# Optimization experiments

Measured on AMD Instinct MI355X. Metric: run time of the kernel, lower is better.

The kernel has to match this reference:

```python
import jax, jax.numpy as jnp
import numpy as np

B = 4096
D_IN = 1024
H1 = 2048
H2 = 1024
E = 7          # num_experts, forced by broadcasting in source
T = 2          # num_tasks
NS = 7         # scene dimension of S
EMB_ROWS = 10
EMB_DIM = 16


def setup_inputs() -> dict:
    key = jax.random.key(0)
    ks = jax.random.split(key, 8)
    x = jax.random.normal(ks[0], (B, D_IN), dtype=jnp.float32)
    scene = jax.random.randint(ks[1], (B,), 0, E)
    # Expert MLP params, stacked over experts: Linear(D_IN->H1)+ReLU, Linear(H1->H2)+ReLU
    W1 = jax.random.normal(ks[2], (E, D_IN, H1), dtype=jnp.float32) * (1.0 / np.sqrt(D_IN))
    b1 = jnp.zeros((E, H1), dtype=jnp.float32)
    W2 = jax.random.normal(ks[3], (E, H1, H2), dtype=jnp.float32) * (1.0 / np.sqrt(H1))
    b2 = jnp.zeros((E, H2), dtype=jnp.float32)
    # Routing tensor S: [7, input_dim+16, num_experts] (xavier-like init)
    S = jax.random.normal(ks[4], (NS, D_IN + EMB_DIM, E), dtype=jnp.float32) * 0.02
    scene_emb = jax.random.normal(ks[5], (EMB_ROWS, EMB_DIM), dtype=jnp.float32)
    return {"x": x, "scene": scene, "W1": W1, "b1": b1, "W2": W2, "b2": b2,
            "S": S, "scene_emb": scene_emb}


def _forward(x, scene, W1, b1, W2, b2, S, scene_emb):
    # Experts (vectorized over the E expert MLPs): [B,E,H2]
    h = jax.nn.relu(jnp.einsum('bd,edh->beh', x, W1) + b1)
    experts_out = jax.nn.relu(jnp.einsum('beh,eho->beo', h, W2) + b2)

    se = scene_emb[scene]                       # [B,16]
    xc = jnp.concatenate([x, se], axis=-1)      # [B, D_IN+16]
    G = jnp.einsum('bd,sde->bse', xc, S)        # [B, 7, E]
    G = jnp.transpose(G, (0, 2, 1))             # [B, E, 7]
    G = jax.nn.softmax(G, axis=-1)

    logG = jnp.log(G)                           # [B, E, 7]
    q = jnp.sum(jnp.log(G * 7.0) / 7.0, axis=-1)  # [B, E]

    KG = jnp.eye(E, dtype=x.dtype)
    ses = KG[scene][:, None, :]                 # [B, 1, E]

    _, pi = jax.lax.top_k(jnp.sum(ses * logG, axis=-1), 6)  # [B,6]
    _, qi = jax.lax.top_k(q, 6)                              # [B,6]
    select = ((KG[pi].sum(axis=1) + KG[qi].sum(axis=1)) > 0).astype(x.dtype)  # [B,E]

    gate = jax.nn.softmax(jnp.sum(G * ses, axis=-1), axis=-1) * select  # [B,E]
    out = jnp.einsum('be,bed->bd', gate, experts_out)                    # [B,H2]
    # self.gate ModuleList is unused in the source forward; each task output is identical
    return jnp.stack([out] * T, axis=0)         # [T, B, H2]


def reference(x, scene, W1, b1, W2, b2, S, scene_emb):
    return _forward(x, scene, W1, b1, W2, b2, S, scene_emb)
```

## Files before the change

kernel.cpp:

```cpp
#include <hip/hip_runtime.h>
#include <hip/hip_bf16.h>

typedef unsigned short u16;
typedef __bf16 bf8 __attribute__((ext_vector_type(8)));
typedef float f4 __attribute__((ext_vector_type(4)));

__device__ __forceinline__ u16 f2bf(float f) {
    unsigned int u = __float_as_uint(f);
    u = (u + 0x7fffu + ((u >> 16) & 1u)) >> 16;
    return (u16)u;
}

__device__ __forceinline__ void gload16(const u16* g, u16* l) {
    __builtin_amdgcn_global_load_lds((const __attribute__((address_space(1))) void*)g,
                                     (__attribute__((address_space(3))) void*)l, 16, 0, 0);
}

__global__ void cvt_x_kernel(const float* __restrict__ in, u16* __restrict__ out, int n4) {
    int i = blockIdx.x * blockDim.x + threadIdx.x;
    int stride = gridDim.x * blockDim.x;
    for (; i < n4; i += stride) {
        float4 v = ((const float4*)in)[i];
        ushort4 o;
        o.x = f2bf(v.x); o.y = f2bf(v.y); o.z = f2bf(v.z); o.w = f2bf(v.w);
        ((ushort4*)out)[i] = o;
    }
}

__global__ void transpose_cvt_kernel(const float* __restrict__ in, u16* __restrict__ out,
                                     int R, int C) {
    __shared__ u16 t[64][71];
    int e = blockIdx.z;
    int c0 = blockIdx.x * 64, r0 = blockIdx.y * 64;
    int tid = threadIdx.x;
    const float* ip = in + (size_t)e * R * C;
    u16* op = out + (size_t)e * R * C;
#pragma unroll
    for (int k = 0; k < 16; ++k) {
        int idx = k * 256 + tid;
        int r = idx >> 6, c = idx & 63;
        t[c][r] = f2bf(ip[(size_t)(r0 + r) * C + c0 + c]);
    }
    __syncthreads();
#pragma unroll
    for (int k = 0; k < 8; ++k) {
        int c = k * 8 + (tid >> 5);
        int rr = (tid & 31) * 2;
        ushort2 v = make_ushort2(t[c][rr], t[c][rr + 1]);
        *(ushort2*)(op + (size_t)(c0 + c) * R + r0 + rr) = v;
    }
}

__global__ void transpose_S_kernel(const float* __restrict__ S, float* __restrict__ ST) {
    int idx = blockIdx.x * 256 + threadIdx.x;
    if (idx >= 1040 * 52) return;
    int d = idx / 52, c = idx % 52;
    ST[idx] = (c < 49) ? S[(c / 7) * 7280 + d * 7 + (c % 7)] : 0.f;
}

__global__ void gating_kernel(const float* __restrict__ x, const int* __restrict__ scene,
                              const float* __restrict__ ST, const float* __restrict__ semb,
                              float* __restrict__ gate) {
    __shared__ float xc[4][1040];
    __shared__ float Lsh[4][49];
    int wv = threadIdx.x >> 6, lane = threadIdx.x & 63;
    int row = blockIdx.x * 4 + wv;
    float* xcw = xc[wv];
    const float* xr = x + (size_t)row * 1024;
    for (int d = lane; d < 1024; d += 64) xcw[d] = xr[d];
    int sc = scene[row];
    if (lane < 16) xcw[1024 + lane] = semb[sc * 16 + lane];
    __syncthreads();

    if (lane < 49) {
        const float* STp = ST + lane;
        float a0 = 0.f, a1 = 0.f, a2 = 0.f, a3 = 0.f;
        for (int d = 0; d < 1040; d += 4) {
            a0 += xcw[d]     * STp[d * 52];
            a1 += xcw[d + 1] * STp[d * 52 + 52];
            a2 += xcw[d + 2] * STp[d * 52 + 104];
            a3 += xcw[d + 3] * STp[d * 52 + 156];
        }
        Lsh[wv][lane] = (a0 + a1) + (a2 + a3);
    }
    __syncthreads();

    if (lane == 0) {
        float logG[7][7], Gsc[7], piS[7], qS[7];
        for (int e = 0; e < 7; e++) {
            float L[7];
            float m = -1e30f;
            for (int s = 0; s < 7; s++) { L[s] = Lsh[wv][s * 7 + e]; m = fmaxf(m, L[s]); }
            float sum = 0.f;
            for (int s = 0; s < 7; s++) sum += expf(L[s] - m);
            float lse = m + logf(sum);
            float qs = 0.f;
            for (int s = 0; s < 7; s++) { logG[e][s] = L[s] - lse; qs += logG[e][s]; }
            piS[e] = logG[e][sc];
            qS[e] = qs;
            Gsc[e] = expf(logG[e][sc]);
        }
        int epi = 0, eqi = 0; float bp = piS[0], bq = qS[0];
        for (int e = 1; e < 7; e++) {
            if (piS[e] <= bp) { bp = piS[e]; epi = e; }
            if (qS[e]  <= bq) { bq = qS[e];  eqi = e; }
        }
        float mg = -1e30f;
        for (int e = 0; e < 7; e++) mg = fmaxf(mg, Gsc[e]);
        float sum = 0.f;
        float ex[7];
        for (int e = 0; e < 7; e++) { ex[e] = expf(Gsc[e] - mg); sum += ex[e]; }
        float inv = 1.f / sum;
        for (int e = 0; e < 7; e++) {
            float g = ex[e] * inv;
            if (e == epi && e == eqi) g = 0.f;
            gate[row * 7 + e] = g;
        }
    }
}

template<bool G2>
__global__ __launch_bounds__(512, 2) void gemm8p_kernel(
    const u16* __restrict__ Abase, const u16* __restrict__ Bbase,
    const float* __restrict__ bias, const float* __restrict__ gate,
    void* __restrict__ outp)
{
    constexpr int M = 4096;
    constexpr int K = G2 ? 2048 : 1024;
    constexpr int N = G2 ? 1024 : 2048;
    constexpr int NT = K / 64;
    constexpr int LOG2NT = G2 ? 5 : 4;

    extern __shared__ u16 lds[];

    const int tid = threadIdx.x;
    const int lane = tid & 63;
    const int wid = tid >> 6;
    const int wr = wid >> 2, wc = wid & 3;
    const int ln15 = lane & 15, lnk = (lane >> 4) * 8;

    int bm, bn, e0, nE, grp;
    if constexpr (G2) {
        int id = blockIdx.x;
        int xcd = id & 7, slot = id >> 3;
        grp = xcd & 1;
        bn = slot & 3;
        bm = (slot >> 2) * 4 + (xcd >> 1);
        e0 = grp * 4; nE = grp ? 3 : 4;
    } else {
        int id = blockIdx.x;
        e0 = id >> 8;
        bm = (id & 255) >> 3;
        bn = id & 7;
        nE = 1; grp = 0;
    }
    const int NTtot = nE * NT;

    const int sr = tid >> 3;
    const int sc = (tid & 7) * 8;

    auto stageA = [&](int gt, int buf) {
#pragma unroll
        for (int l = 0; l < 2; ++l) {
            int r = l * 64 + sr;
            int cs = sc ^ ((r & 7) << 3);
            const u16* g = Abase + (G2 ? (size_t)(e0 + (gt >> LOG2NT)) * M * K : (size_t)0)
                         + (size_t)(bm * 128 + r) * K + (gt & (NT - 1)) * 64 + cs;
            gload16(g, lds + buf * 24576 + l * 4096 + tid * 8);
        }
    };
    auto stageB = [&](int gt, int buf, int h) {
#pragma unroll
        for (int l = 0; l < 2; ++l) {
            int rb = h * 128 + l * 64 + sr;
            int cs = sc ^ ((rb & 7) << 3);
            const u16* g = Bbase + (size_t)(e0 + (gt >> LOG2NT)) * N * K
                         + (size_t)(bn * 256 + rb) * K + (gt & (NT - 1)) * 64 + cs;
            gload16(g, lds + buf * 24576 + 8192 + h * 8192 + l * 4096 + tid * 8);
        }
    };
    auto aoff = [&](int mi, int ks) {
        int r = wr * 64 + mi * 16 + ln15;
        int c = ks * 32 + lnk;
        return r * 64 + (c ^ ((r & 7) << 3));
    };
    auto boff = [&](int ni, int ks) {
        int rb = wc * 64 + ni * 16 + ln15;
        int c = ks * 32 + lnk;
        return rb * 64 + (c ^ ((rb & 7) << 3));
    };

    f4 acc[4][4] = {};
    f4 fin[4][4] = {};
    bf8 aA[2][2], bL[2][2], bH[2][2];

    stageA(0, 0); stageB(0, 0, 0); stageB(0, 0, 1);

    for (int gt = 0; gt < NTtot; ++gt) {
        const int cur = gt & 1, nxt = cur ^ 1;
        const bool more = (gt + 1 < NTtot);
        const u16* Ac = lds + cur * 24576;
        const u16* Bc = lds + cur * 24576 + 8192;
        if (more) {
            stageA(gt + 1, nxt); stageB(gt + 1, nxt, 0);
            asm volatile("s_waitcnt vmcnt(4)" ::: "memory");
        } else {
            asm volatile("s_waitcnt vmcnt(0)" ::: "memory");
        }
        __builtin_amdgcn_sched_barrier(0);
        __builtin_amdgcn_s_barrier();
        __builtin_amdgcn_sched_barrier(0);
#pragma unroll
        for (int mi = 0; mi < 2; ++mi)
#pragma unroll
            for (int ks = 0; ks < 2; ++ks)
                aA[mi][ks] = *(const bf8*)(Ac + aoff(mi, ks));
#pragma unroll
        for (int ni = 0; ni < 2; ++ni)
#pragma unroll
            for (int ks = 0; ks < 2; ++ks)
                bL[ni][ks] = *(const bf8*)(Bc + boff(ni, ks));
        asm volatile("s_waitcnt lgkmcnt(0)" ::: "memory");
        __builtin_amdgcn_sched_barrier(0);
        __builtin_amdgcn_s_setprio(1);
#pragma unroll
        for (int mi = 0; mi < 2; ++mi)
#pragma unroll
            for (int ni = 0; ni < 2; ++ni)
#pragma unroll
                for (int ks = 0; ks < 2; ++ks)
                    acc[mi][ni] = __builtin_amdgcn_mfma_f32_16x16x32_bf16(aA[mi][ks], bL[ni][ks], acc[mi][ni], 0, 0, 0);
        __builtin_amdgcn_s_setprio(0);
        if (more) stageB(gt + 1, nxt, 1);
#pragma unroll
        for (int ni = 0; ni < 2; ++ni)
#pragma unroll
            for (int ks = 0; ks < 2; ++ks)
                bH[ni][ks] = *(const bf8*)(Bc + boff(2 + ni, ks));
        asm volatile("s_waitcnt lgkmcnt(0)" ::: "memory");
        __builtin_amdgcn_sched_barrier(0);
        __builtin_amdgcn_s_setprio(1);
#pragma unroll
        for (int mi = 0; mi < 2; ++mi)
#pragma unroll
            for (int ni = 0; ni < 2; ++ni)
#pragma unroll
                for (int ks = 0; ks < 2; ++ks)
                    acc[mi][2 + ni] = __builtin_amdgcn_mfma_f32_16x16x32_bf16(aA[mi][ks], bH[ni][ks], acc[mi][2 + ni], 0, 0, 0);
        __builtin_amdgcn_s_setprio(0);
#pragma unroll
        for (int mi = 0; mi < 2; ++mi)
#pragma unroll
            for (int ks = 0; ks < 2; ++ks)
                aA[mi][ks] = *(const bf8*)(Ac + aoff(2 + mi, ks));
        asm volatile("s_waitcnt lgkmcnt(0)" ::: "memory");
        __builtin_amdgcn_sched_barrier(0);
        __builtin_amdgcn_s_setprio(1);
#pragma unroll
        for (int mi = 0; mi < 2; ++mi)
#pragma unroll
            for (int ni = 0; ni < 2; ++ni)
#pragma unroll
                for (int ks = 0; ks < 2; ++ks)
                    acc[2 + mi][2 + ni] = __builtin_amdgcn_mfma_f32_16x16x32_bf16(aA[mi][ks], bH[ni][ks], acc[2 + mi][2 + ni], 0, 0, 0);
        __builtin_amdgcn_s_setprio(0);
        __builtin_amdgcn_sched_barrier(0);
        __builtin_amdgcn_s_barrier();
        __builtin_amdgcn_sched_barrier(0);
        __builtin_amdgcn_s_setprio(1);
#pragma unroll
        for (int mi = 0; mi < 2; ++mi)
#pragma unroll
            for (int ni = 0; ni < 2; ++ni)
#pragma unroll
                for (int ks = 0; ks < 2; ++ks)
                    acc[2 + mi][ni] = __builtin_amdgcn_mfma_f32_16x16x32_bf16(aA[mi][ks], bL[ni][ks], acc[2 + mi][ni], 0, 0, 0);
        __builtin_amdgcn_s_setprio(0);
        __builtin_amdgcn_sched_barrier(0);
        if constexpr (G2) {
            if ((gt & (NT - 1)) == NT - 1) {
                int e = e0 + (gt >> LOG2NT);
                float bloc[4];
#pragma unroll
                for (int ni = 0; ni < 4; ++ni)
                    bloc[ni] = bias[e * N + bn * 256 + wc * 64 + ni * 16 + ln15];
#pragma unroll
                for (int mi = 0; mi < 4; ++mi)
#pragma unroll
                    for (int i = 0; i < 4; ++i) {
                        int row = bm * 128 + wr * 64 + mi * 16 + (lane >> 4) * 4 + i;
                        float g = gate[row * 7 + e];
#pragma unroll
                        for (int ni = 0; ni < 4; ++ni) {
                            fin[mi][ni][i] += g * fmaxf(acc[mi][ni][i] + bloc[ni], 0.f);
                            acc[mi][ni][i] = 0.f;
                        }
                    }
            }
        }
    }

    if constexpr (G2) {
        float* po = (float*)outp + (size_t)grp * M * N;
#pragma unroll
        for (int mi = 0; mi < 4; ++mi)
#pragma unroll
            for (int i = 0; i < 4; ++i) {
                size_t row = (size_t)(bm * 128 + wr * 64 + mi * 16 + (lane >> 4) * 4 + i);
#pragma unroll
                for (int ni = 0; ni < 4; ++ni)
                    po[row * N + bn * 256 + wc * 64 + ni * 16 + ln15] = fin[mi][ni][i];
            }
    } else {
        float bloc[4];
#pragma unroll
        for (int ni = 0; ni < 4; ++ni)
            bloc[ni] = bias[e0 * N + bn * 256 + wc * 64 + ni * 16 + ln15];
        u16* Hp = (u16*)outp + (size_t)e0 * M * N;
#pragma unroll
        for (int mi = 0; mi < 4; ++mi)
#pragma unroll
            for (int i = 0; i < 4; ++i) {
                size_t row = (size_t)(bm * 128 + wr * 64 + mi * 16 + (lane >> 4) * 4 + i);
#pragma unroll
                for (int ni = 0; ni < 4; ++ni) {
                    __builtin_nontemporal_store(
                        f2bf(fmaxf(acc[mi][ni][i] + bloc[ni], 0.f)),
                        &Hp[row * N + bn * 256 + wc * 64 + ni * 16 + ln15]);
                }
            }
    }
}

__global__ void combine_kernel(const float* __restrict__ p0, const float* __restrict__ p1,
                               float* __restrict__ out, int n4) {
    int i = blockIdx.x * blockDim.x + threadIdx.x;
    int stride = gridDim.x * blockDim.x;
    for (; i < n4; i += stride) {
        float4 a = ((const float4*)p0)[i];
        float4 b = ((const float4*)p1)[i];
        float4 v = make_float4(a.x + b.x, a.y + b.y, a.z + b.z, a.w + b.w);
        ((float4*)out)[i] = v;
        ((float4*)out)[i + n4] = v;
    }
}

extern "C" void kernel_launch(void* const* d_in, const int* in_sizes, int n_in,
                              void* d_out, int out_size, void* d_ws, size_t ws_size,
                              hipStream_t stream) {
    const float* x     = (const float*)d_in[0];
    const int*   scene = (const int*)d_in[1];
    const float* W1    = (const float*)d_in[2];
    const float* b1    = (const float*)d_in[3];
    const float* W2    = (const float*)d_in[4];
    const float* b2    = (const float*)d_in[5];
    const float* S     = (const float*)d_in[6];
    const float* semb  = (const float*)d_in[7];
    float* out = (float*)d_out;

    char* ws = (char*)d_ws;
    float* part = (float*)(ws);
    u16*   xb   = (u16*)(ws);
    u16*   W1T  = (u16*)(ws + 8388608);
    u16*   W2T  = (u16*)(ws + 37748736);
    u16*   Hb   = (u16*)(ws + 67108864);
    float* gate = (float*)(ws + 184549376);
    float* ST   = (float*)(ws + 184664064);

    (void)hipFuncSetAttribute(reinterpret_cast<const void*>(gemm8p_kernel<false>),
                              hipFuncAttributeMaxDynamicSharedMemorySize, 98304);
    (void)hipFuncSetAttribute(reinterpret_cast<const void*>(gemm8p_kernel<true>),
                              hipFuncAttributeMaxDynamicSharedMemorySize, 98304);

    cvt_x_kernel<<<2048, 256, 0, stream>>>(x, xb, 4096 * 1024 / 4);
    transpose_cvt_kernel<<<dim3(32, 16, 7), 256, 0, stream>>>(W1, W1T, 1024, 2048);
    transpose_cvt_kernel<<<dim3(16, 32, 7), 256, 0, stream>>>(W2, W2T, 2048, 1024);
    transpose_S_kernel<<<(1040 * 52 + 255) / 256, 256, 0, stream>>>(S, ST);
    gating_kernel<<<1024, 256, 0, stream>>>(x, scene, ST, semb, gate);
    gemm8p_kernel<false><<<1792, 512, 98304, stream>>>(xb, W1T, b1, nullptr, Hb);
    gemm8p_kernel<true><<<256, 512, 98304, stream>>>(Hb, W2T, b2, gate, part);
    combine_kernel<<<2048, 256, 0, stream>>>(part, part + 4096 * 1024, out, 4096 * 1024 / 4);
}
```

Baseline: 381.2 us.

## Use 128x128 GEMM tiles and split expert reduction with atomic accumulation

Both GEMMs move from 512-thread 128x256 tiles to 256-thread 128x128 tiles, with an XCD-aware block remapping. The second GEMM no longer loops over groups of 3 or 4 experts per block. It now launches one block per (expert, tile) and reduces gated outputs into a zeroed fp32 buffer with atomicAdd, so the combine kernel only copies. The aim is finer-grained parallelism and a fix for the 4-versus-3 expert imbalance between block groups. In exchange it adds a memset, many float atomics with up to 7-way contention per element, and less A/B reuse per tile.

```diff
diff --git a/kernel.cpp b/kernel.cpp
--- a/kernel.cpp
+++ b/kernel.cpp
@@ -120,7 +120,7 @@
 }
 
 template<bool G2>
-__global__ __launch_bounds__(512, 2) void gemm8p_kernel(
+__global__ __launch_bounds__(256, 2) void gemm128_kernel(
     const u16* __restrict__ Abase, const u16* __restrict__ Bbase,
     const float* __restrict__ bias, const float* __restrict__ gate,
     void* __restrict__ outp)
@@ -129,54 +129,50 @@
     constexpr int K = G2 ? 2048 : 1024;
     constexpr int N = G2 ? 1024 : 2048;
     constexpr int NT = K / 64;
-    constexpr int LOG2NT = G2 ? 5 : 4;
 
     extern __shared__ u16 lds[];
 
     const int tid = threadIdx.x;
     const int lane = tid & 63;
     const int wid = tid >> 6;
-    const int wr = wid >> 2, wc = wid & 3;
+    const int wr = wid >> 1, wc = wid & 1;
     const int ln15 = lane & 15, lnk = (lane >> 4) * 8;
 
-    int bm, bn, e0, nE, grp;
+    const int nwg = gridDim.x, cpx = nwg >> 3;
+    const int id = (blockIdx.x & 7) * cpx + (blockIdx.x >> 3);
+    int e0, bm, bn;
     if constexpr (G2) {
-        int id = blockIdx.x;
-        int xcd = id & 7, slot = id >> 3;
-        grp = xcd & 1;
-        bn = slot & 3;
-        bm = (slot >> 2) * 4 + (xcd >> 1);
-        e0 = grp * 4; nE = grp ? 3 : 4;
-    } else {
-        int id = blockIdx.x;
         e0 = id >> 8;
         bm = (id & 255) >> 3;
         bn = id & 7;
-        nE = 1; grp = 0;
-    }
-    const int NTtot = nE * NT;
+    } else {
+        e0 = id >> 9;
+        bm = (id & 511) >> 4;
+        bn = id & 15;
+    }
+
+    const u16* Ae = Abase + (G2 ? (size_t)e0 * M * K : (size_t)0);
+    const u16* Be = Bbase + (size_t)e0 * N * K;
 
     const int sr = tid >> 3;
     const int sc = (tid & 7) * 8;
 
-    auto stageA = [&](int gt, int buf) {
+    auto stageA = [&](int kt, int buf) {
+#pragma unroll
+        for (int l = 0; l < 4; ++l) {
+            int r = l * 32 + sr;
+            int cs = sc ^ ((r & 7) << 3);
+            const u16* g = Ae + (size_t)(bm * 128 + r) * K + kt * 64 + cs;
+            gload16(g, lds + buf * 16384 + l * 2048 + tid * 8);
+        }
+    };
+    auto stageB = [&](int kt, int buf, int h) {
 #pragma unroll
         for (int l = 0; l < 2; ++l) {
-            int r = l * 64 + sr;
-            int cs = sc ^ ((r & 7) << 3);
-            const u16* g = Abase + (G2 ? (size_t)(e0 + (gt >> LOG2NT)) * M * K : (size_t)0)
-                         + (size_t)(bm * 128 + r) * K + (gt & (NT - 1)) * 64 + cs;
-            gload16(g, lds + buf * 24576 + l * 4096 + tid * 8);
-        }
-    };
-    auto stageB = [&](int gt, int buf, int h) {
-#pragma unroll
-        for (int l = 0; l < 2; ++l) {
-            int rb = h * 128 + l * 64 + sr;
+            int rb = h * 64 + l * 32 + sr;
             int cs = sc ^ ((rb & 7) << 3);
-            const u16* g = Bbase + (size_t)(e0 + (gt >> LOG2NT)) * N * K
-                         + (size_t)(bn * 256 + rb) * K + (gt & (NT - 1)) * 64 + cs;
-            gload16(g, lds + buf * 24576 + 8192 + h * 8192 + l * 4096 + tid * 8);
+            const u16* g = Be + (size_t)(bn * 128 + rb) * K + kt * 64 + cs;
+            gload16(g, lds + buf * 16384 + 8192 + h * 4096 + l * 2048 + tid * 8);
         }
     };
     auto aoff = [&](int mi, int ks) {
@@ -191,19 +187,18 @@
     };
 
     f4 acc[4][4] = {};
-    f4 fin[4][4] = {};
     bf8 aA[2][2], bL[2][2], bH[2][2];
 
     stageA(0, 0); stageB(0, 0, 0); stageB(0, 0, 1);
 
-    for (int gt = 0; gt < NTtot; ++gt) {
+    for (int gt = 0; gt < NT; ++gt) {
         const int cur = gt & 1, nxt = cur ^ 1;
-        const bool more = (gt + 1 < NTtot);
-        const u16* Ac = lds + cur * 24576;
-        const u16* Bc = lds + cur * 24576 + 8192;
+        const bool more = (gt + 1 < NT);
+        const u16* Ac = lds + cur * 16384;
+        const u16* Bc = lds + cur * 16384 + 8192;
         if (more) {
             stageA(gt + 1, nxt); stageB(gt + 1, nxt, 0);
-            asm volatile("s_waitcnt vmcnt(4)" ::: "memory");
+            asm volatile("s_waitcnt vmcnt(6)" ::: "memory");
         } else {
             asm volatile("s_waitcnt vmcnt(0)" ::: "memory");
         }
@@ -277,45 +272,27 @@
                     acc[2 + mi][ni] = __builtin_amdgcn_mfma_f32_16x16x32_bf16(aA[mi][ks], bL[ni][ks], acc[2 + mi][ni], 0, 0, 0);
         __builtin_amdgcn_s_setprio(0);
         __builtin_amdgcn_sched_barrier(0);
-        if constexpr (G2) {
-            if ((gt & (NT - 1)) == NT - 1) {
-                int e = e0 + (gt >> LOG2NT);
-                float bloc[4];
-#pragma unroll
-                for (int ni = 0; ni < 4; ++ni)
-                    bloc[ni] = bias[e * N + bn * 256 + wc * 64 + ni * 16 + ln15];
-#pragma unroll
-                for (int mi = 0; mi < 4; ++mi)
-#pragma unroll
-                    for (int i = 0; i < 4; ++i) {
-                        int row = bm * 128 + wr * 64 + mi * 16 + (lane >> 4) * 4 + i;
-                        float g = gate[row * 7 + e];
-#pragma unroll
-                        for (int ni = 0; ni < 4; ++ni) {
-                            fin[mi][ni][i] += g * fmaxf(acc[mi][ni][i] + bloc[ni], 0.f);
-                            acc[mi][ni][i] = 0.f;
-                        }
-                    }
-            }
-        }
-    }
-
+    }
+
+    float bloc[4];
+#pragma unroll
+    for (int ni = 0; ni < 4; ++ni)
+        bloc[ni] = bias[e0 * N + bn * 128 + wc * 64 + ni * 16 + ln15];
     if constexpr (G2) {
-        float* po = (float*)outp + (size_t)grp * M * N;
+        float* part = (float*)outp;
 #pragma unroll
         for (int mi = 0; mi < 4; ++mi)
 #pragma unroll
             for (int i = 0; i < 4; ++i) {
-                size_t row = (size_t)(bm * 128 + wr * 64 + mi * 16 + (lane >> 4) * 4 + i);
-#pragma unroll
-                for (int ni = 0; ni < 4; ++ni)
-                    po[row * N + bn * 256 + wc * 64 + ni * 16 + ln15] = fin[mi][ni][i];
+                int row = bm * 128 + wr * 64 + mi * 16 + (lane >> 4) * 4 + i;
+                float g = gate[row * 7 + e0];
+#pragma unroll
+                for (int ni = 0; ni < 4; ++ni) {
+                    float v = g * fmaxf(acc[mi][ni][i] + bloc[ni], 0.f);
+                    atomicAdd(&part[(size_t)row * N + bn * 128 + wc * 64 + ni * 16 + ln15], v);
+                }
             }
     } else {
-        float bloc[4];
-#pragma unroll
-        for (int ni = 0; ni < 4; ++ni)
-            bloc[ni] = bias[e0 * N + bn * 256 + wc * 64 + ni * 16 + ln15];
         u16* Hp = (u16*)outp + (size_t)e0 * M * N;
 #pragma unroll
         for (int mi = 0; mi < 4; ++mi)
@@ -326,20 +303,17 @@
                 for (int ni = 0; ni < 4; ++ni) {
                     __builtin_nontemporal_store(
                         f2bf(fmaxf(acc[mi][ni][i] + bloc[ni], 0.f)),
-                        &Hp[row * N + bn * 256 + wc * 64 + ni * 16 + ln15]);
+                        &Hp[row * N + bn * 128 + wc * 64 + ni * 16 + ln15]);
                 }
             }
     }
 }
 
-__global__ void combine_kernel(const float* __restrict__ p0, const float* __restrict__ p1,
-                               float* __restrict__ out, int n4) {
+__global__ void combine_kernel(const float* __restrict__ part, float* __restrict__ out, int n4) {
     int i = blockIdx.x * blockDim.x + threadIdx.x;
     int stride = gridDim.x * blockDim.x;
     for (; i < n4; i += stride) {
-        float4 a = ((const float4*)p0)[i];
-        float4 b = ((const float4*)p1)[i];
-        float4 v = make_float4(a.x + b.x, a.y + b.y, a.z + b.z, a.w + b.w);
+        float4 v = ((const float4*)part)[i];
         ((float4*)out)[i] = v;
         ((float4*)out)[i + n4] = v;
     }
@@ -367,17 +341,18 @@
     float* gate = (float*)(ws + 184549376);
     float* ST   = (float*)(ws + 184664064);
 
-    (void)hipFuncSetAttribute(reinterpret_cast<const void*>(gemm8p_kernel<false>),
-                              hipFuncAttributeMaxDynamicSharedMemorySize, 98304);
-    (void)hipFuncSetAttribute(reinterpret_cast<const void*>(gemm8p_kernel<true>),
-                              hipFuncAttributeMaxDynamicSharedMemorySize, 98304);
+    (void)hipFuncSetAttribute(reinterpret_cast<const void*>(gemm128_kernel<false>),
+                              hipFuncAttributeMaxDynamicSharedMemorySize, 65536);
+    (void)hipFuncSetAttribute(reinterpret_cast<const void*>(gemm128_kernel<true>),
+                              hipFuncAttributeMaxDynamicSharedMemorySize, 65536);
 
     cvt_x_kernel<<<2048, 256, 0, stream>>>(x, xb, 4096 * 1024 / 4);
     transpose_cvt_kernel<<<dim3(32, 16, 7), 256, 0, stream>>>(W1, W1T, 1024, 2048);
     transpose_cvt_kernel<<<dim3(16, 32, 7), 256, 0, stream>>>(W2, W2T, 2048, 1024);
     transpose_S_kernel<<<(1040 * 52 + 255) / 256, 256, 0, stream>>>(S, ST);
     gating_kernel<<<1024, 256, 0, stream>>>(x, scene, ST, semb, gate);
-    gemm8p_kernel<false><<<1792, 512, 98304, stream>>>(xb, W1T, b1, nullptr, Hb);
-    gemm8p_kernel<true><<<256, 512, 98304, stream>>>(Hb, W2T, b2, gate, part);
-    combine_kernel<<<2048, 256, 0, stream>>>(part, part + 4096 * 1024, out, 4096 * 1024 / 4);
-}
+    gemm128_kernel<false><<<3584, 256, 65536, stream>>>(xb, W1T, b1, nullptr, Hb);
+    (void)hipMemsetAsync(part, 0, (size_t)4096 * 1024 * 4, stream);
+    gemm128_kernel<true><<<1792, 256, 65536, stream>>>(Hb, W2T, b2, gate, part);
+    combine_kernel<<<2048, 256, 0, stream>>>(part, out, 4096 * 1024 / 4);
+}
```

Result: slower. 408.6 us (+7.2%).

## Fuse x bf16 conversion into gating and replace combine pass with atomic adds

Applied to the files above, without the earlier changes.

The float-to-bf16 conversion of x moves into the gating kernel, which already loads each row into LDS, so the separate conversion launch and its extra read of x go away. The two expert-group partial outputs are now accumulated directly into the zeroed output, both task copies, with float atomicAdd. This removes the partial buffer and the combine kernel. It adds a memset, twice as many atomic writes in the GEMM2 epilogue, and a summation order that is no longer deterministic.

```diff
diff --git a/kernel.cpp b/kernel.cpp
--- a/kernel.cpp
+++ b/kernel.cpp
@@ -14,17 +14,6 @@
 __device__ __forceinline__ void gload16(const u16* g, u16* l) {
     __builtin_amdgcn_global_load_lds((const __attribute__((address_space(1))) void*)g,
                                      (__attribute__((address_space(3))) void*)l, 16, 0, 0);
-}
-
-__global__ void cvt_x_kernel(const float* __restrict__ in, u16* __restrict__ out, int n4) {
-    int i = blockIdx.x * blockDim.x + threadIdx.x;
-    int stride = gridDim.x * blockDim.x;
-    for (; i < n4; i += stride) {
-        float4 v = ((const float4*)in)[i];
-        ushort4 o;
-        o.x = f2bf(v.x); o.y = f2bf(v.y); o.z = f2bf(v.z); o.w = f2bf(v.w);
-        ((ushort4*)out)[i] = o;
-    }
 }
 
 __global__ void transpose_cvt_kernel(const float* __restrict__ in, u16* __restrict__ out,
@@ -60,7 +49,7 @@
 
 __global__ void gating_kernel(const float* __restrict__ x, const int* __restrict__ scene,
                               const float* __restrict__ ST, const float* __restrict__ semb,
-                              float* __restrict__ gate) {
+                              float* __restrict__ gate, u16* __restrict__ xb) {
     __shared__ float xc[4][1040];
     __shared__ float Lsh[4][49];
     int wv = threadIdx.x >> 6, lane = threadIdx.x & 63;
@@ -71,6 +60,14 @@
     int sc = scene[row];
     if (lane < 16) xcw[1024 + lane] = semb[sc * 16 + lane];
     __syncthreads();
+
+    u16* xrow = xb + (size_t)row * 1024;
+    for (int d = lane * 4; d < 1024; d += 256) {
+        ushort4 o;
+        o.x = f2bf(xcw[d]);     o.y = f2bf(xcw[d + 1]);
+        o.z = f2bf(xcw[d + 2]); o.w = f2bf(xcw[d + 3]);
+        *(ushort4*)(xrow + d) = o;
+    }
 
     if (lane < 49) {
         const float* STp = ST + lane;
@@ -139,11 +136,11 @@
     const int wr = wid >> 2, wc = wid & 3;
     const int ln15 = lane & 15, lnk = (lane >> 4) * 8;
 
-    int bm, bn, e0, nE, grp;
+    int bm, bn, e0, nE;
     if constexpr (G2) {
         int id = blockIdx.x;
         int xcd = id & 7, slot = id >> 3;
-        grp = xcd & 1;
+        int grp = xcd & 1;
         bn = slot & 3;
         bm = (slot >> 2) * 4 + (xcd >> 1);
         e0 = grp * 4; nE = grp ? 3 : 4;
@@ -152,7 +149,7 @@
         e0 = id >> 8;
         bm = (id & 255) >> 3;
         bn = id & 7;
-        nE = 1; grp = 0;
+        nE = 1;
     }
     const int NTtot = nE * NT;
 
@@ -301,15 +298,19 @@
     }
 
     if constexpr (G2) {
-        float* po = (float*)outp + (size_t)grp * M * N;
+        float* po = (float*)outp;
 #pragma unroll
         for (int mi = 0; mi < 4; ++mi)
 #pragma unroll
             for (int i = 0; i < 4; ++i) {
                 size_t row = (size_t)(bm * 128 + wr * 64 + mi * 16 + (lane >> 4) * 4 + i);
 #pragma unroll
-                for (int ni = 0; ni < 4; ++ni)
-                    po[row * N + bn * 256 + wc * 64 + ni * 16 + ln15] = fin[mi][ni][i];
+                for (int ni = 0; ni < 4; ++ni) {
+                    size_t idx = row * N + bn * 256 + wc * 64 + ni * 16 + ln15;
+                    float v = fin[mi][ni][i];
+                    atomicAdd(&po[idx], v);
+                    atomicAdd(&po[(size_t)M * N + idx], v);
+                }
             }
     } else {
         float bloc[4];
@@ -329,19 +330,6 @@
                         &Hp[row * N + bn * 256 + wc * 64 + ni * 16 + ln15]);
                 }
             }
-    }
-}
-
-__global__ void combine_kernel(const float* __restrict__ p0, const float* __restrict__ p1,
-                               float* __restrict__ out, int n4) {
-    int i = blockIdx.x * blockDim.x + threadIdx.x;
-    int stride = gridDim.x * blockDim.x;
-    for (; i < n4; i += stride) {
-        float4 a = ((const float4*)p0)[i];
-        float4 b = ((const float4*)p1)[i];
-        float4 v = make_float4(a.x + b.x, a.y + b.y, a.z + b.z, a.w + b.w);
-        ((float4*)out)[i] = v;
-        ((float4*)out)[i + n4] = v;
     }
 }
 
@@ -359,7 +347,6 @@
     float* out = (float*)d_out;
 
     char* ws = (char*)d_ws;
-    float* part = (float*)(ws);
     u16*   xb   = (u16*)(ws);
     u16*   W1T  = (u16*)(ws + 8388608);
     u16*   W2T  = (u16*)(ws + 37748736);
@@ -372,12 +359,11 @@
     (void)hipFuncSetAttribute(reinterpret_cast<const void*>(gemm8p_kernel<true>),
                               hipFuncAttributeMaxDynamicSharedMemorySize, 98304);
 
-    cvt_x_kernel<<<2048, 256, 0, stream>>>(x, xb, 4096 * 1024 / 4);
     transpose_cvt_kernel<<<dim3(32, 16, 7), 256, 0, stream>>>(W1, W1T, 1024, 2048);
     transpose_cvt_kernel<<<dim3(16, 32, 7), 256, 0, stream>>>(W2, W2T, 2048, 1024);
     transpose_S_kernel<<<(1040 * 52 + 255) / 256, 256, 0, stream>>>(S, ST);
-    gating_kernel<<<1024, 256, 0, stream>>>(x, scene, ST, semb, gate);
+    gating_kernel<<<1024, 256, 0, stream>>>(x, scene, ST, semb, gate, xb);
     gemm8p_kernel<false><<<1792, 512, 98304, stream>>>(xb, W1T, b1, nullptr, Hb);
-    gemm8p_kernel<true><<<256, 512, 98304, stream>>>(Hb, W2T, b2, gate, part);
-    combine_kernel<<<2048, 256, 0, stream>>>(part, part + 4096 * 1024, out, 4096 * 1024 / 4);
-}
+    (void)hipMemsetAsync(out, 0, (size_t)2 * 4096 * 1024 * 4, stream);
+    gemm8p_kernel<true><<<256, 512, 98304, stream>>>(Hb, W2T, b2, gate, out);
+}
```

After: 410.5 us. 7.7% more time.
